# Kernel tuning notes

Measured on AMD Instinct MI355X. Metric: run time of the kernel, lower is better.

The kernel has to match this reference:

```python
import jax, jax.numpy as jnp
import numpy as np

B, C, T = 16, 768, 1024
STEPS, NNEG, OFFSET = 12, 10, 1
COPIES = NNEG + 1


def setup_inputs() -> dict:
    key = jax.random.key(0)
    k1, k2, k3, k4 = jax.random.split(key, 4)
    x = jax.random.normal(k1, (B, C, T), jnp.float32)
    y = jax.random.normal(k2, (B, C, T), jnp.float32)
    # ConvTranspose2d(in_dim, out_dim, (1, steps)) weight -> [C_in, C_out, steps]
    W = jax.random.normal(k3, (C, C, STEPS), jnp.float32) * 0.02
    b = jnp.zeros((C,), jnp.float32)
    # Negative-sample indices, replicating torch sample_negatives (sample_distance=None):
    # randint in [0, T-1), bump collisions with the positive timestep, add per-batch offset.
    neg = jax.random.randint(k4, (B, NNEG * T), 0, T - 1)
    tszs = jnp.repeat(jnp.arange(T), NNEG)  # [NNEG*T]
    neg = jnp.where(neg >= tszs[None, :], neg + 1, neg)
    neg = neg + jnp.arange(B)[:, None] * T  # index into flattened [B*T]
    return {"x": x, "y": y, "W": W, "b": b, "neg_idxs": neg}


def reference(x, y, W, b, neg_idxs):
    # project_to_steps: ConvTranspose2d with kernel (1, STEPS) on [B,C,T,1] -> [B,C,T,STEPS]
    proj = jnp.einsum('bct,cds->bdts', x, W) + b[None, :, None, None]

    # gather negatives: y -> [C, B*T], fancy-index, reshape to [NNEG, B, C, T]
    yf = jnp.transpose(y, (1, 0, 2)).reshape(C, B * T)
    negs = yf[:, neg_idxs.reshape(-1)].reshape(C, B, NNEG, T)
    negs = jnp.transpose(negs, (2, 1, 0, 3))  # [NNEG, B, C, T]

    targets = jnp.concatenate([y[None], negs], axis=0)  # [COPIES, B, C, T]

    steps = min(STEPS, T - OFFSET)
    preds = []
    for i in range(steps):  # small fixed loop over prediction steps (ragged slice sizes)
        off = i + OFFSET
        # [T-off, B, COPIES]: dot context at step i with targets shifted by off
        p = jnp.einsum('bct,nbct->tbn', proj[..., :T - off, i], targets[..., off:])
        preds.append(p.reshape(-1))
    predictions = jnp.concatenate(preds).reshape(-1, COPIES)  # infonce logits
    labels = jnp.zeros((predictions.shape[0],), jnp.int32)  # positive is copy 0
    return predictions, labels
```

## Files before the change

kernel.cpp:

```cpp
#include <hip/hip_runtime.h>

typedef __bf16 bf16;
typedef __attribute__((ext_vector_type(8))) __bf16 bf16x8;
typedef __attribute__((ext_vector_type(4))) __bf16 bf16x4;
typedef __attribute__((ext_vector_type(4))) float f32x4;

#define B_ 16
#define C_ 768
#define T_ 1024
#define S_ 12
#define NNEG_ 10
#define NCOPY 11
#define NPRED_ROWS 195360
#define NPRED (NPRED_ROWS * NCOPY)
#define NT_ 12

__device__ __forceinline__ void gload16(const void* g, void* l) {
    __builtin_amdgcn_global_load_lds(
        (__attribute__((address_space(1))) void*)g,
        (__attribute__((address_space(3))) void*)l, 16, 0, 0);
}

__global__ void k_wt(const float* __restrict__ W, bf16* __restrict__ WtT) {
    int id = blockIdx.x * blockDim.x + threadIdx.x;
    if (id >= C_ * C_) return;
    int d = id / C_, c = id % C_;
    const float* src = W + ((size_t)c * C_ + d) * S_;
#pragma unroll
    for (int s = 0; s < S_; ++s)
        WtT[(size_t)s * C_ * C_ + id] = (bf16)src[s];
}

__global__ void k_tr2(const float* __restrict__ x, const float* __restrict__ y,
                      bf16* __restrict__ xTc, bf16* __restrict__ yTc, int b0, int cb) {
    __shared__ float tile[32][33];
    int zz = blockIdx.z;
    const float* src = (zz < cb) ? x : y;
    bf16* dst = (zz < cb) ? xTc : yTc;
    int bb = (zz < cb) ? zz : zz - cb;
    int b = b0 + bb;
    int c0 = blockIdx.y * 32, t0 = blockIdx.x * 32;
    int tx = threadIdx.x & 31, ty = threadIdx.x >> 5;
#pragma unroll
    for (int i = 0; i < 4; ++i)
        tile[ty + i * 8][tx] = src[((size_t)b * C_ + c0 + ty + i * 8) * T_ + t0 + tx];
    __syncthreads();
#pragma unroll
    for (int i = 0; i < 4; ++i)
        dst[((size_t)bb * T_ + t0 + ty + i * 8) * C_ + c0 + tx] = (bf16)tile[tx][ty + i * 8];
}

#define SBAR()  __builtin_amdgcn_s_barrier()
#define SCHED() __builtin_amdgcn_sched_barrier(0)
#define LGKM0() asm volatile("s_waitcnt lgkmcnt(0)" ::: "memory")

__global__ __launch_bounds__(512, 2) void k_gemm8(
    const bf16* __restrict__ xTc, const bf16* __restrict__ WtT,
    const float* __restrict__ bias, bf16* __restrict__ P)
{
    const int nblk = blockIdx.x;
    const int tblk = blockIdx.y;
    const int bb   = blockIdx.z;

    const int tid  = threadIdx.x;
    const int wv   = tid >> 6, lane = tid & 63;
    const int mwz  = wv >> 2, nwz = wv & 3;
    const int quad = lane >> 4, l15 = lane & 15;

    __shared__ __align__(16) bf16 sA[2][256][64];
    __shared__ __align__(16) bf16 sB[2][256][64];

    const int lrow = lane >> 3;
    const int laneOff = lrow * 1536 + (((lane & 7) * 16) ^ (lrow << 4));
    const char* aG = (const char*)(WtT + (size_t)(nblk * 256) * C_) + laneOff;
    const char* bG = (const char*)(xTc + ((size_t)bb * T_ + tblk * 256) * C_) + laneOff;
    const int h0 = wv * 16, h1 = wv * 16 + 8;
    const int arw0 = (h0 & 63) + ((h0 >> 6) << 7);
    const int arw1 = (h1 & 63) + ((h1 >> 6) << 7);
    const int brw0 = (h0 & 31) + ((h0 >> 5) << 6);
    const int brw1 = (h1 & 31) + ((h1 >> 5) << 6);

#define STAGE_A(bufn, roff, kt) do { \
    gload16(aG + (size_t)(arw0 + (roff)) * 1536 + (kt) * 128, &sA[bufn][arw0 + (roff)][0]); \
    gload16(aG + (size_t)(arw1 + (roff)) * 1536 + (kt) * 128, &sA[bufn][arw1 + (roff)][0]); \
} while (0)
#define STAGE_B(bufn, roff, kt) do { \
    gload16(bG + (size_t)(brw0 + (roff)) * 1536 + (kt) * 128, &sB[bufn][brw0 + (roff)][0]); \
    gload16(bG + (size_t)(brw1 + (roff)) * 1536 + (kt) * 128, &sB[bufn][brw1 + (roff)][0]); \
} while (0)

    const int csw0 = (quad * 16) ^ ((l15 & 7) << 4);
    const int csw1 = (64 + quad * 16) ^ ((l15 & 7) << 4);
    const char* aRd0 = (const char*)&sA[0][mwz * 128 + l15][0] + csw0;
    const char* aRd1 = (const char*)&sA[0][mwz * 128 + l15][0] + csw1;
    const char* bRd0 = (const char*)&sB[0][nwz * 64 + l15][0] + csw0;
    const char* bRd1 = (const char*)&sB[0][nwz * 64 + l15][0] + csw1;

    f32x4 acc[8][4] = {};

    STAGE_A(0, 0, 0);
    STAGE_A(0, 64, 0);
    STAGE_B(0, 32, 0);
    STAGE_B(0, 0, 0);
    STAGE_A(1, 0, 1);
    STAGE_B(1, 32, 1);
    STAGE_A(1, 64, 1);
    asm volatile("s_waitcnt vmcnt(6)" ::: "memory");
    SCHED(); SBAR(); SCHED();

#pragma unroll 2
    for (int j = 0; j < NT_; ++j) {
        const int cur = j & 1;
        const int coff = cur << 15;
        const char* aC0 = aRd0 + coff; const char* aC1 = aRd1 + coff;
        const char* bC0 = bRd0 + coff; const char* bC1 = bRd1 + coff;

        bf16x8 a03[4][2], a47[4][2], b01[2][2], b23[2][2], b01p[2][2];

        if (j + 1 < NT_) STAGE_B(cur ^ 1, 0, j + 1);
#pragma unroll
        for (int i = 0; i < 4; ++i) {
            a03[i][0] = *(const bf16x8*)(aC0 + i * 2048);
            a03[i][1] = *(const bf16x8*)(aC1 + i * 2048);
        }
#pragma unroll
        for (int i = 0; i < 2; ++i) {
            b01[i][0] = *(const bf16x8*)(bC0 + i * 2048);
            b01[i][1] = *(const bf16x8*)(bC1 + i * 2048);
        }
        SCHED(); SBAR(); LGKM0(); SCHED();
        __builtin_amdgcn_s_setprio(1);
#pragma unroll
        for (int i = 0; i < 4; ++i)
#pragma unroll
            for (int n = 0; n < 2; ++n)
#pragma unroll
                for (int kk = 0; kk < 2; ++kk)
                    acc[i][n] = __builtin_amdgcn_mfma_f32_16x16x32_bf16(a03[i][kk], b01[n][kk], acc[i][n], 0, 0, 0);
        __builtin_amdgcn_s_setprio(0);
        SCHED(); SBAR(); SCHED();

        if (j + 2 < NT_) STAGE_A(cur, 0, j + 2);
#pragma unroll
        for (int i = 0; i < 2; ++i) {
            b23[i][0] = *(const bf16x8*)(bC0 + 4096 + i * 2048);
            b23[i][1] = *(const bf16x8*)(bC1 + 4096 + i * 2048);
        }
        SCHED(); SBAR(); LGKM0(); SCHED();
        __builtin_amdgcn_s_setprio(1);
#pragma unroll
        for (int i = 0; i < 4; ++i)
#pragma unroll
            for (int n = 0; n < 2; ++n)
#pragma unroll
                for (int kk = 0; kk < 2; ++kk)
                    acc[i][2 + n] = __builtin_amdgcn_mfma_f32_16x16x32_bf16(a03[i][kk], b23[n][kk], acc[i][2 + n], 0, 0, 0);
        __builtin_amdgcn_s_setprio(0);
        SCHED(); SBAR(); SCHED();

        if (j + 2 < NT_) STAGE_B(cur, 32, j + 2);
#pragma unroll
        for (int i = 0; i < 4; ++i) {
            a47[i][0] = *(const bf16x8*)(aC0 + 8192 + i * 2048);
            a47[i][1] = *(const bf16x8*)(aC1 + 8192 + i * 2048);
        }
        SCHED(); SBAR(); LGKM0(); SCHED();
        __builtin_amdgcn_s_setprio(1);
#pragma unroll
        for (int i = 0; i < 4; ++i)
#pragma unroll
            for (int n = 0; n < 2; ++n)
#pragma unroll
                for (int kk = 0; kk < 2; ++kk)
                    acc[4 + i][2 + n] = __builtin_amdgcn_mfma_f32_16x16x32_bf16(a47[i][kk], b23[n][kk], acc[4 + i][2 + n], 0, 0, 0);
        __builtin_amdgcn_s_setprio(0);
        SCHED(); SBAR(); SCHED();

        if (j + 2 < NT_) STAGE_A(cur, 64, j + 2);
#pragma unroll
        for (int i = 0; i < 2; ++i) {
            b01p[i][0] = *(const bf16x8*)(bC0 + i * 2048);
            b01p[i][1] = *(const bf16x8*)(bC1 + i * 2048);
        }
        if (j < NT_ - 2)       { asm volatile("s_waitcnt vmcnt(6)" ::: "memory"); }
        else if (j == NT_ - 2) { asm volatile("s_waitcnt vmcnt(0)" ::: "memory"); }
        SCHED(); SBAR(); LGKM0(); SCHED();
        __builtin_amdgcn_s_setprio(1);
#pragma unroll
        for (int i = 0; i < 4; ++i)
#pragma unroll
            for (int n = 0; n < 2; ++n)
#pragma unroll
                for (int kk = 0; kk < 2; ++kk)
                    acc[4 + i][n] = __builtin_amdgcn_mfma_f32_16x16x32_bf16(a47[i][kk], b01p[n][kk], acc[4 + i][n], 0, 0, 0);
        __builtin_amdgcn_s_setprio(0);
        SCHED(); SBAR(); SCHED();
    }

    const size_t SC = (size_t)S_ * C_;
    bf16* Pb = P + ((size_t)bb * T_) * SC;
#pragma unroll
    for (int i = 0; i < 8; ++i) {
        const int nloc = mwz * 128 + i * 16 + quad * 4;
        const f32x4 bv = *(const f32x4*)&bias[(nblk % 3) * 256 + nloc];
#pragma unroll
        for (int n = 0; n < 4; ++n) {
            const int t = tblk * 256 + nwz * 64 + n * 16 + l15;
            bf16x4 v;
#pragma unroll
            for (int r = 0; r < 4; ++r) v[r] = (bf16)(acc[i][n][r] + bv[r]);
            *(bf16x4*)&Pb[(size_t)t * SC + nblk * 256 + nloc] = v;
        }
    }
#undef STAGE_A
#undef STAGE_B
}

__global__ __launch_bounds__(256, 4) void k_pred(
    const bf16* __restrict__ P, const bf16* __restrict__ yTc,
    const int* __restrict__ neg, float* __restrict__ out, int b0)
{
    const int widx = blockIdx.x;
    const int bb = widx >> 10, tp = widx & 1023;
    const int b = b0 + bb;
    const int tid = threadIdx.x;

    __shared__ __align__(16) char sAB[24 * 1536];

#pragma unroll
    for (int i = 0; i < 18; ++i) {
        int idx = i * 256 + tid;
        int row = idx / 192;
        int off = (idx % 192) * 8;
        const bf16* grow;
        if (row < 12) {
            int tA = tp - 1 - row; if (tA < 0) tA = 0;
            grow = P + ((size_t)bb * T_ + tA) * (S_ * C_) + row * C_;
        } else {
            int n = row - 12;
            int ridx;
            if (n == 0 || n >= NCOPY) ridx = bb * T_ + tp;
            else ridx = neg[(size_t)b * (NNEG_ * T_) + (n - 1) * T_ + tp] - b0 * T_;
            grow = yTc + (size_t)ridx * C_;
        }
        uint2 v = *(const uint2*)((const char*)grow + off);
        int sb = (((off >> 4) << 4) ^ ((row & 7) << 4)) | (off & 8);
        *(uint2*)(&sAB[row * 1536 + sb]) = v;
    }
    __syncthreads();

    if (tid >= 64) return;
    const int lane = tid;
    const int quad = lane >> 4, l15 = lane & 15;

    const int ra = l15 < 12 ? l15 : 11;
    const int rb = 12 + (l15 < 12 ? l15 : 11);
    const char* pa = sAB + ra * 1536;
    const char* pb = sAB + rb * 1536;
    const int xa = (ra & 7) << 4, xb = (rb & 7) << 4;

    f32x4 acc = {};
#pragma unroll
    for (int kt = 0; kt < 24; ++kt) {
        const int col = ((kt << 2) + quad) << 4;
        bf16x8 av = *(const bf16x8*)(pa + (col ^ xa));
        bf16x8 bv = *(const bf16x8*)(pb + (col ^ xb));
        acc = __builtin_amdgcn_mfma_f32_16x16x32_bf16(av, bv, acc, 0, 0, 0);
    }

#pragma unroll
    for (int r = 0; r < 4; ++r) {
        int s = quad * 4 + r;
        int t = tp - 1 - s;
        if (s < S_ && t >= 0) {
            int rowbase = s * (T_ - 1) - (s * (s - 1)) / 2;
            size_t row = (size_t)(rowbase + t) * B_ + b;
            if (l15 < NCOPY)       out[row * NCOPY + l15] = acc[r];
            else if (l15 == NCOPY) out[NPRED + row] = 0.0f;
        }
    }
}

extern "C" void kernel_launch(void* const* d_in, const int* in_sizes, int n_in,
                              void* d_out, int out_size, void* d_ws, size_t ws_size,
                              hipStream_t stream) {
    const float* x    = (const float*)d_in[0];
    const float* y    = (const float*)d_in[1];
    const float* W    = (const float*)d_in[2];
    const float* bias = (const float*)d_in[3];
    const int*   neg  = (const int*)d_in[4];
    float* out = (float*)d_out;

    const size_t offW    = (size_t)S_ * C_ * C_ * 2;
    const size_t perb_xy = (size_t)T_ * C_ * 2;
    const size_t perb_p  = (size_t)T_ * S_ * C_ * 2;
    const size_t perb    = 2 * perb_xy + perb_p;

    int bchunk = (int)((ws_size - offW) / perb);
    if (bchunk < 1) bchunk = 1;
    if (bchunk > B_) bchunk = B_;

    char* ws = (char*)d_ws;
    bf16* WtT = (bf16*)ws;
    bf16* xTc = (bf16*)(ws + offW);
    bf16* yTc = (bf16*)(ws + offW + (size_t)bchunk * perb_xy);
    bf16* P   = (bf16*)(ws + offW + (size_t)bchunk * perb_xy * 2);

    k_wt<<<dim3((C_ * C_ + 255) / 256), 256, 0, stream>>>(W, WtT);

    for (int b0 = 0; b0 < B_;) {
        int cb = bchunk < (B_ - b0) ? bchunk : (B_ - b0);
        k_tr2<<<dim3(T_ / 32, C_ / 32, 2 * cb), 256, 0, stream>>>(x, y, xTc, yTc, b0, cb);
        k_gemm8<<<dim3(36, 4, cb), 512, 0, stream>>>(xTc, WtT, bias, P);
        k_pred<<<dim3(cb << 10), 256, 0, stream>>>(P, yTc, neg, out, b0);
        b0 += cb;
    }
}
```

Baseline: 653.3 us.

## Store projections pre-shifted by step so pred kernel reads one contiguous row

The GEMM epilogue now writes each projection step s to time row t+s+1 in a padded [T+S] buffer, so the prediction kernel reads one contiguous 12*C row per timestep instead of 12 scattered rows. Negative indices are loaded once into shared memory, and the P stores and loads use nontemporal hints. The weight-transpose kernel is rewritten to stage through LDS for coalesced reads and writes. This adds workspace padding. Padded rows that are never written may be read for the boundary cases, which assumes the final output masking ignores them.

Result: slower. 777.1 us (+18.9%).

```diff
diff --git a/kernel.cpp b/kernel.cpp
--- a/kernel.cpp
+++ b/kernel.cpp
@@ -9,6 +9,7 @@
 #define C_ 768
 #define T_ 1024
 #define S_ 12
+#define TP_ (T_ + S_)
 #define NNEG_ 10
 #define NCOPY 11
 #define NPRED_ROWS 195360
@@ -21,14 +22,24 @@
         (__attribute__((address_space(3))) void*)l, 16, 0, 0);
 }
 
-__global__ void k_wt(const float* __restrict__ W, bf16* __restrict__ WtT) {
-    int id = blockIdx.x * blockDim.x + threadIdx.x;
-    if (id >= C_ * C_) return;
-    int d = id / C_, c = id % C_;
-    const float* src = W + ((size_t)c * C_ + d) * S_;
-#pragma unroll
-    for (int s = 0; s < S_; ++s)
-        WtT[(size_t)s * C_ * C_ + id] = (bf16)src[s];
+__global__ __launch_bounds__(256) void k_wt(const float* __restrict__ W, bf16* __restrict__ WtT) {
+    __shared__ float sW[32 * 385];
+    const int c0 = blockIdx.x * 32, d0 = blockIdx.y * 32;
+    const int tid = threadIdx.x;
+#pragma unroll 4
+    for (int k = 0; k < 48; ++k) {
+        int idx = k * 256 + tid;
+        int c = idx / 384, r = idx % 384;
+        sW[c * 385 + r] = W[((size_t)(c0 + c) * C_ + d0) * S_ + r];
+    }
+    __syncthreads();
+#pragma unroll 4
+    for (int k = 0; k < 48; ++k) {
+        int idx = k * 256 + tid;
+        int row = idx >> 5, c = idx & 31;
+        int s = row >> 5, d = row & 31;
+        WtT[((size_t)s * C_ + d0 + d) * C_ + c0 + c] = (bf16)sW[c * 385 + d * 12 + s];
+    }
 }
 
 __global__ void k_tr2(const float* __restrict__ x, const float* __restrict__ y,
@@ -198,18 +209,21 @@
     }
 
     const size_t SC = (size_t)S_ * C_;
-    bf16* Pb = P + ((size_t)bb * T_) * SC;
+    const int sblk = nblk / 3;
+    const int dblk = (nblk % 3) * 256;
+    bf16* Pb = P + (size_t)bb * TP_ * SC + (size_t)sblk * C_ + dblk;
 #pragma unroll
     for (int i = 0; i < 8; ++i) {
         const int nloc = mwz * 128 + i * 16 + quad * 4;
-        const f32x4 bv = *(const f32x4*)&bias[(nblk % 3) * 256 + nloc];
+        const f32x4 bv = *(const f32x4*)&bias[dblk + nloc];
 #pragma unroll
         for (int n = 0; n < 4; ++n) {
             const int t = tblk * 256 + nwz * 64 + n * 16 + l15;
+            const int tp = t + sblk + 1;
             bf16x4 v;
 #pragma unroll
             for (int r = 0; r < 4; ++r) v[r] = (bf16)(acc[i][n][r] + bv[r]);
-            *(bf16x4*)&Pb[(size_t)t * SC + nblk * 256 + nloc] = v;
+            __builtin_nontemporal_store(v, (bf16x4*)&Pb[(size_t)tp * SC + nloc]);
         }
     }
 #undef STAGE_A
@@ -226,26 +240,30 @@
     const int tid = threadIdx.x;
 
     __shared__ __align__(16) char sAB[24 * 1536];
-
+    __shared__ int sRid[12];
+
+    if (tid < 12) {
+        int ridx;
+        if (tid == 0) ridx = bb * T_ + tp;
+        else ridx = neg[(size_t)b * (NNEG_ * T_) + (tid - 1) * T_ + tp] - b0 * T_;
+        sRid[tid] = ridx;
+    }
+    __syncthreads();
+
+    const char* Prow = (const char*)(P + ((size_t)bb * TP_ + tp) * (S_ * C_));
 #pragma unroll
     for (int i = 0; i < 18; ++i) {
         int idx = i * 256 + tid;
         int row = idx / 192;
         int off = (idx % 192) * 8;
-        const bf16* grow;
+        unsigned long long v;
         if (row < 12) {
-            int tA = tp - 1 - row; if (tA < 0) tA = 0;
-            grow = P + ((size_t)bb * T_ + tA) * (S_ * C_) + row * C_;
+            v = __builtin_nontemporal_load((const unsigned long long*)(Prow + idx * 8));
         } else {
-            int n = row - 12;
-            int ridx;
-            if (n == 0 || n >= NCOPY) ridx = bb * T_ + tp;
-            else ridx = neg[(size_t)b * (NNEG_ * T_) + (n - 1) * T_ + tp] - b0 * T_;
-            grow = yTc + (size_t)ridx * C_;
-        }
-        uint2 v = *(const uint2*)((const char*)grow + off);
-        int sb = (((off >> 4) << 4) ^ ((row & 7) << 4)) | (off & 8);
-        *(uint2*)(&sAB[row * 1536 + sb]) = v;
+            v = *(const unsigned long long*)((const char*)(yTc + (size_t)sRid[row - 12] * C_) + off);
+        }
+        int sb = ((off & ~15) ^ ((row & 7) << 4)) | (off & 8);
+        *(unsigned long long*)(&sAB[row * 1536 + sb]) = v;
     }
     __syncthreads();
 
@@ -293,7 +311,7 @@
 
     const size_t offW    = (size_t)S_ * C_ * C_ * 2;
     const size_t perb_xy = (size_t)T_ * C_ * 2;
-    const size_t perb_p  = (size_t)T_ * S_ * C_ * 2;
+    const size_t perb_p  = (size_t)TP_ * S_ * C_ * 2;
     const size_t perb    = 2 * perb_xy + perb_p;
 
     int bchunk = (int)((ws_size - offW) / perb);
@@ -306,7 +324,7 @@
     bf16* yTc = (bf16*)(ws + offW + (size_t)bchunk * perb_xy);
     bf16* P   = (bf16*)(ws + offW + (size_t)bchunk * perb_xy * 2);
 
-    k_wt<<<dim3((C_ * C_ + 255) / 256), 256, 0, stream>>>(W, WtT);
+    k_wt<<<dim3(C_ / 32, C_ / 32), 256, 0, stream>>>(W, WtT);
 
     for (int b0 = 0; b0 < B_;) {
         int cb = bchunk < (B_ - b0) ? bchunk : (B_ - b0);
```
